# Kernel optimization log

Hardware: AMD Instinct MI355X
Metric: run time of the kernel (lower is better)

The kernel has to match this reference:

```python
import jax, jax.numpy as jnp
import numpy as np
from jax import lax

B, T, I, H, O = 1024, 2048, 16, 64, 1
V_TH = 1.0


def setup_inputs() -> dict:
    key = jax.random.key(0)
    ks = jax.random.split(key, 6)
    x = jax.random.normal(ks[0], (B, T, I), dtype=jnp.float32)
    W1 = jax.random.normal(ks[1], (H, I), dtype=jnp.float32) * 0.1
    b1 = jnp.zeros((H,), dtype=jnp.float32)
    # somatic heterogeneity: half slow, half fast time constants
    tau_lo = jax.random.uniform(ks[2], (H // 2,), minval=0.0, maxval=2.0, dtype=jnp.float32)
    tau_hi = jax.random.uniform(ks[3], (H - H // 2,), minval=3.0, maxval=6.0, dtype=jnp.float32)
    tau_m = jnp.concatenate([tau_lo, tau_hi])
    W2 = jax.random.normal(ks[4], (O, H), dtype=jnp.float32) * 0.1
    b2 = jnp.zeros((O,), dtype=jnp.float32)
    return {"x": x, "W1": W1, "b1": b1, "tau_m": tau_m, "W2": W2, "b2": b2}


def reference(x, W1, b1, tau_m, W2, b2):
    Bn, Tn, _ = x.shape
    Hn = W1.shape[0]
    # precompute fc1 projection for all timesteps: [T, B, H]
    ic = jnp.einsum('bti,hi->tbh', x, W1) + b1
    alpha = jax.nn.sigmoid(tau_m)  # [H]

    def step(carry, ic_t):
        v, s = carry
        v = alpha * v + (1.0 - alpha) * ic_t - V_TH * s
        s = (v - V_TH > 0).astype(v.dtype)
        return (v, s), s

    init = (jnp.zeros((Bn, Hn), x.dtype), jnp.zeros((Bn, Hn), x.dtype))
    _, spikes = lax.scan(step, init, ic)  # spikes: [T, B, H]
    integrated = spikes[Tn // 2:].sum(axis=0)  # [B, H]
    return integrated @ W2.T + b2
```

## Files before the change

### kernel.cpp

```cpp
#include <hip/hip_runtime.h>


constexpr int Bn = 1024;
constexpr int Tn = 2048;
constexpr int In = 16;
constexpr int Hn = 64;

constexpr int CHUNK = 128;
constexpr int NCH = Tn / CHUNK;
constexpr int CHUNK_F4 = CHUNK * In / 4;
constexpr int F4_PER_LANE = CHUNK_F4 / 64;

__global__ __launch_bounds__(64) void snn_fused_kernel(
    const float* __restrict__ x,
    const float* __restrict__ W1,
    const float* __restrict__ b1,
    const float* __restrict__ tau,
    const float* __restrict__ W2,
    const float* __restrict__ b2,
    float* __restrict__ out)
{
    const int b = blockIdx.x;
    const int lane = threadIdx.x;

    __shared__ float lds[2][CHUNK * In];

    float w[In];
#pragma unroll
    for (int i = 0; i < In; ++i) w[i] = W1[lane * In + i];
    const float bias = b1[lane];

    const double td = (double)tau[lane];
    const float alpha = (float)(1.0 / (1.0 + exp(-td)));
    const float onem = __fsub_rn(1.0f, alpha);

    const float4* xg = (const float4*)(x + (size_t)b * (size_t)(Tn * In));

    float4 st[F4_PER_LANE];
#pragma unroll
    for (int j = 0; j < F4_PER_LANE; ++j) st[j] = xg[j * 64 + lane];
#pragma unroll
    for (int j = 0; j < F4_PER_LANE; ++j)
        ((float4*)lds[0])[j * 64 + lane] = st[j];

    float v = 0.0f, s = 0.0f, acc = 0.0f;

    for (int c = 0; c < NCH; ++c) {
        const int cur = c & 1;

        if (c + 1 < NCH) {
#pragma unroll
            for (int j = 0; j < F4_PER_LANE; ++j)
                st[j] = xg[(c + 1) * CHUNK_F4 + j * 64 + lane];
        }

        const float* xt = lds[cur];
        const bool second = (c >= NCH / 2);

#pragma unroll 4
        for (int tt = 0; tt < CHUNK; ++tt) {
            const float4* xr = (const float4*)(xt + tt * In);
            const float4 x0 = xr[0];
            const float4 x1 = xr[1];
            const float4 x2 = xr[2];
            const float4 x3 = xr[3];

            float ic;
            ic = __fmul_rn(x0.x, w[0]);
            ic = __fadd_rn(ic, __fmul_rn(x0.y, w[1]));
            ic = __fadd_rn(ic, __fmul_rn(x0.z, w[2]));
            ic = __fadd_rn(ic, __fmul_rn(x0.w, w[3]));
            ic = __fadd_rn(ic, __fmul_rn(x1.x, w[4]));
            ic = __fadd_rn(ic, __fmul_rn(x1.y, w[5]));
            ic = __fadd_rn(ic, __fmul_rn(x1.z, w[6]));
            ic = __fadd_rn(ic, __fmul_rn(x1.w, w[7]));
            ic = __fadd_rn(ic, __fmul_rn(x2.x, w[8]));
            ic = __fadd_rn(ic, __fmul_rn(x2.y, w[9]));
            ic = __fadd_rn(ic, __fmul_rn(x2.z, w[10]));
            ic = __fadd_rn(ic, __fmul_rn(x2.w, w[11]));
            ic = __fadd_rn(ic, __fmul_rn(x3.x, w[12]));
            ic = __fadd_rn(ic, __fmul_rn(x3.y, w[13]));
            ic = __fadd_rn(ic, __fmul_rn(x3.z, w[14]));
            ic = __fadd_rn(ic, __fmul_rn(x3.w, w[15]));
            ic = __fadd_rn(ic, bias);

            const float t1 = __fmul_rn(alpha, v);
            const float t2 = __fmul_rn(onem, ic);
            v = __fsub_rn(__fadd_rn(t1, t2), s);

            s = (__fsub_rn(v, 1.0f) > 0.0f) ? 1.0f : 0.0f;

            if (second) acc = __fadd_rn(acc, s);
        }

        if (c + 1 < NCH) {
#pragma unroll
            for (int j = 0; j < F4_PER_LANE; ++j)
                ((float4*)lds[cur ^ 1])[j * 64 + lane] = st[j];
        }
    }

    float val = __fmul_rn(acc, W2[lane]);
#pragma unroll
    for (int off = 32; off > 0; off >>= 1)
        val = __fadd_rn(val, __shfl_down(val, off));
    if (lane == 0) out[b] = __fadd_rn(val, b2[0]);
}

extern "C" void kernel_launch(void* const* d_in, const int* in_sizes, int n_in,
                              void* d_out, int out_size, void* d_ws, size_t ws_size,
                              hipStream_t stream) {
    const float* x   = (const float*)d_in[0];
    const float* W1  = (const float*)d_in[1];
    const float* b1  = (const float*)d_in[2];
    const float* tau = (const float*)d_in[3];
    const float* W2  = (const float*)d_in[4];
    const float* b2  = (const float*)d_in[5];
    float* out = (float*)d_out;

    snn_fused_kernel<<<dim3(Bn), dim3(64), 0, stream>>>(x, W1, b1, tau, W2, b2, out);
}
```

Baseline: 341.4 us.

## Transpose LDS tile and compute two timesteps with packed float2 math

Stores each chunk of x in shared memory transposed (feature-major, with padded rows) so a lane can read a float2 covering two consecutive timesteps per feature. The input projection then runs on packed two-wide vectors (v_pk_mul/v_pk_add) with fp contraction off to keep rounding bitwise identical, which roughly halves the VALU instructions for the dot product. The recurrence stays serial. In exchange, the LDS writes become scalar scattered stores, and the padding may or may not avoid bank conflicts.

```diff
diff --git a/kernel.cpp b/kernel.cpp
--- a/kernel.cpp
+++ b/kernel.cpp
@@ -1,13 +1,15 @@
 #include <hip/hip_runtime.h>
 
+
+typedef float v2f __attribute__((ext_vector_type(2)));
 
 constexpr int Bn = 1024;
 constexpr int Tn = 2048;
 constexpr int In = 16;
-constexpr int Hn = 64;
 
 constexpr int CHUNK = 128;
 constexpr int NCH = Tn / CHUNK;
+constexpr int ROWP = CHUNK + 2;
 constexpr int CHUNK_F4 = CHUNK * In / 4;
 constexpr int F4_PER_LANE = CHUNK_F4 / 64;
 
@@ -23,12 +25,16 @@
     const int b = blockIdx.x;
     const int lane = threadIdx.x;
 
-    __shared__ float lds[2][CHUNK * In];
+    __shared__ float lds[2][In * ROWP];
 
-    float w[In];
+    v2f w2[In];
 #pragma unroll
-    for (int i = 0; i < In; ++i) w[i] = W1[lane * In + i];
-    const float bias = b1[lane];
+    for (int i = 0; i < In; ++i) {
+        const float wv = W1[lane * In + i];
+        w2[i].x = wv; w2[i].y = wv;
+    }
+    const float biasf = b1[lane];
+    v2f bias2; bias2.x = biasf; bias2.y = biasf;
 
     const double td = (double)tau[lane];
     const float alpha = (float)(1.0 / (1.0 + exp(-td)));
@@ -36,12 +42,24 @@
 
     const float4* xg = (const float4*)(x + (size_t)b * (size_t)(Tn * In));
 
+    int wbase[4];
+#pragma unroll
+    for (int c = 0; c < 4; ++c) {
+        const int d0 = lane * 4 + c;
+        wbase[c] = (d0 & 15) * ROWP + (d0 >> 4);
+    }
+
     float4 st[F4_PER_LANE];
+
 #pragma unroll
     for (int j = 0; j < F4_PER_LANE; ++j) st[j] = xg[j * 64 + lane];
 #pragma unroll
-    for (int j = 0; j < F4_PER_LANE; ++j)
-        ((float4*)lds[0])[j * 64 + lane] = st[j];
+    for (int j = 0; j < F4_PER_LANE; ++j) {
+        lds[0][wbase[0] + j * 16] = st[j].x;
+        lds[0][wbase[1] + j * 16] = st[j].y;
+        lds[0][wbase[2] + j * 16] = st[j].z;
+        lds[0][wbase[3] + j * 16] = st[j].w;
+    }
 
     float v = 0.0f, s = 0.0f, acc = 0.0f;
 
@@ -58,45 +76,39 @@
         const bool second = (c >= NCH / 2);
 
 #pragma unroll 4
-        for (int tt = 0; tt < CHUNK; ++tt) {
-            const float4* xr = (const float4*)(xt + tt * In);
-            const float4 x0 = xr[0];
-            const float4 x1 = xr[1];
-            const float4 x2 = xr[2];
-            const float4 x3 = xr[3];
+        for (int tt = 0; tt < CHUNK; tt += 2) {
+#pragma clang fp contract(off)
+            v2f a2 = (*(const v2f*)&xt[0 * ROWP + tt]) * w2[0];
+#pragma unroll
+            for (int i = 1; i < In; ++i)
+                a2 = a2 + (*(const v2f*)&xt[i * ROWP + tt]) * w2[i];
+            const v2f ic2 = a2 + bias2;
 
-            float ic;
-            ic = __fmul_rn(x0.x, w[0]);
-            ic = __fadd_rn(ic, __fmul_rn(x0.y, w[1]));
-            ic = __fadd_rn(ic, __fmul_rn(x0.z, w[2]));
-            ic = __fadd_rn(ic, __fmul_rn(x0.w, w[3]));
-            ic = __fadd_rn(ic, __fmul_rn(x1.x, w[4]));
-            ic = __fadd_rn(ic, __fmul_rn(x1.y, w[5]));
-            ic = __fadd_rn(ic, __fmul_rn(x1.z, w[6]));
-            ic = __fadd_rn(ic, __fmul_rn(x1.w, w[7]));
-            ic = __fadd_rn(ic, __fmul_rn(x2.x, w[8]));
-            ic = __fadd_rn(ic, __fmul_rn(x2.y, w[9]));
-            ic = __fadd_rn(ic, __fmul_rn(x2.z, w[10]));
-            ic = __fadd_rn(ic, __fmul_rn(x2.w, w[11]));
-            ic = __fadd_rn(ic, __fmul_rn(x3.x, w[12]));
-            ic = __fadd_rn(ic, __fmul_rn(x3.y, w[13]));
-            ic = __fadd_rn(ic, __fmul_rn(x3.z, w[14]));
-            ic = __fadd_rn(ic, __fmul_rn(x3.w, w[15]));
-            ic = __fadd_rn(ic, bias);
-
-            const float t1 = __fmul_rn(alpha, v);
-            const float t2 = __fmul_rn(onem, ic);
-            v = __fsub_rn(__fadd_rn(t1, t2), s);
-
-            s = (__fsub_rn(v, 1.0f) > 0.0f) ? 1.0f : 0.0f;
-
-            if (second) acc = __fadd_rn(acc, s);
+            {
+                const float t1 = __fmul_rn(alpha, v);
+                const float t2 = __fmul_rn(onem, ic2.x);
+                v = __fsub_rn(__fadd_rn(t1, t2), s);
+                s = (__fsub_rn(v, 1.0f) > 0.0f) ? 1.0f : 0.0f;
+                if (second) acc = __fadd_rn(acc, s);
+            }
+            {
+                const float t1 = __fmul_rn(alpha, v);
+                const float t2 = __fmul_rn(onem, ic2.y);
+                v = __fsub_rn(__fadd_rn(t1, t2), s);
+                s = (__fsub_rn(v, 1.0f) > 0.0f) ? 1.0f : 0.0f;
+                if (second) acc = __fadd_rn(acc, s);
+            }
         }
 
         if (c + 1 < NCH) {
+            float* dst = lds[cur ^ 1];
 #pragma unroll
-            for (int j = 0; j < F4_PER_LANE; ++j)
-                ((float4*)lds[cur ^ 1])[j * 64 + lane] = st[j];
+            for (int j = 0; j < F4_PER_LANE; ++j) {
+                dst[wbase[0] + j * 16] = st[j].x;
+                dst[wbase[1] + j * 16] = st[j].y;
+                dst[wbase[2] + j * 16] = st[j].z;
+                dst[wbase[3] + j * 16] = st[j].w;
+            }
         }
     }
 
```

Measured after the change: 319.4 us. -6.5%, faster.
